# Kernel optimization log

Hardware: AMD Instinct MI355X
Metric: run time of the kernel (lower is better)

Reference implementation:

```python
import jax, jax.numpy as jnp
import numpy as np

N = 50000
E = 800000
IN_F = 128
OUT_F = 128


def setup_inputs() -> dict:
    key = jax.random.key(0)
    k1, k2, k3, k4, k5 = jax.random.split(key, 5)
    x = jax.random.normal(k1, (N, IN_F), dtype=jnp.float32)
    # sparse adjacency as COO edge list: row = dst (aggregating node), col = src
    edge_index = jax.random.randint(k2, (2, E), 0, N, dtype=jnp.int64)
    edge_weight = jax.random.uniform(k3, (E,), dtype=jnp.float32)
    # nn.Linear(in_features, out_features): W is [out, in], b is [out]
    W = jax.random.normal(k4, (OUT_F, IN_F), dtype=jnp.float32) * (1.0 / np.sqrt(IN_F))
    b = jax.random.normal(k5, (OUT_F,), dtype=jnp.float32) * 0.01
    return {"x": x, "edge_index": edge_index, "edge_weight": edge_weight, "W": W, "b": b}


def reference(x, edge_index, edge_weight, W, b):
    # hidden = self.linear(x)  -> [N, out]
    hidden = jnp.einsum("ni,oi->no", x, W) + b
    # out = adj @ hidden (SpMM): out[dst] += w_e * hidden[src]
    dst = edge_index[0]
    src = edge_index[1]
    msgs = edge_weight[:, None] * hidden[src]  # [E, out]
    out = jax.ops.segment_sum(msgs, dst, num_segments=x.shape[0])
    return out
```

## Files before the change

kernel.cpp:

```cpp
#include <hip/hip_runtime.h>
#include <hip/hip_bf16.h>

#define N_NODES 50000
#define N_EDGES 800000
#define FEAT    128
#define N_TILES (N_NODES / 16)
#define MAXD    32
#define OVF_CAP 16384
#define NODES_PER_GRP 6250
#define CHUNK   2048
#define NCHUNK  ((N_EDGES + CHUNK - 1) / CHUNK)

using short8  = __attribute__((ext_vector_type(8))) short;
using float4v = __attribute__((ext_vector_type(4))) float;


__device__ __forceinline__ unsigned short f2b(float f) {
    __hip_bfloat16 h = __float2bfloat16(f);
    return __builtin_bit_cast(unsigned short, h);
}

__global__ void k_init(const int* __restrict__ ei, int* __restrict__ flag,
                       int* __restrict__ fill) {
    int i = blockIdx.x * blockDim.x + threadIdx.x;
    if (i < N_NODES) fill[i] = 0;
    if (blockIdx.x == 0 && threadIdx.x < 64) {
        unsigned long long m = __ballot(ei[2 * threadIdx.x + 1] != 0);
        if (threadIdx.x == 0) { flag[0] = (m == 0ULL) ? 1 : 0; flag[1] = 0; }
    }
}

__global__ __launch_bounds__(256) void k_gemm(const float* __restrict__ x,
                                              const float* __restrict__ W,
                                              const float* __restrict__ bias,
                                              unsigned short* __restrict__ hidden) {
    __shared__ __align__(16) unsigned short Wlds[128 * 136];

    const int t = threadIdx.x;
    for (int j = 0; j < 16; ++j) {
        int idx4 = j * 256 + t;
        float4v wv = *(const float4v*)(W + (size_t)idx4 * 4);
        int r = (idx4 * 4) >> 7;
        int c = (idx4 * 4) & 127;
        unsigned short* p = &Wlds[r * 136 + c];
        p[0] = f2b(wv[0]); p[1] = f2b(wv[1]); p[2] = f2b(wv[2]); p[3] = f2b(wv[3]);
    }
    __syncthreads();

    const int wave = t >> 6;
    const int lane = t & 63;
    int tile = blockIdx.x * 4 + wave;
    if (tile >= N_TILES) tile = N_TILES - 1;
    const int rowBase = tile * 16;
    const int m    = lane & 15;
    const int quad = lane >> 4;

    float4v acc[8];
    for (int i = 0; i < 8; ++i) acc[i] = (float4v){0.f, 0.f, 0.f, 0.f};

    for (int kk = 0; kk < 4; ++kk) {
        const int k0 = kk * 32 + quad * 8;
        const float* ap = x + (size_t)(rowBase + m) * FEAT + k0;
        float4v a0 = *(const float4v*)(ap);
        float4v a1 = *(const float4v*)(ap + 4);
        short8 af;
        for (int j = 0; j < 4; ++j) { af[j] = (short)f2b(a0[j]); af[4 + j] = (short)f2b(a1[j]); }
        for (int nt = 0; nt < 8; ++nt) {
            short8 bf = *(const short8*)&Wlds[(nt * 16 + m) * 136 + k0];
            acc[nt] = __builtin_amdgcn_mfma_f32_16x16x32_bf16(af, bf, acc[nt], 0, 0, 0);
        }
    }

    const int r0 = rowBase + quad * 4;
    for (int nt = 0; nt < 8; ++nt) {
        const int col = nt * 16 + m;
        const float bc = bias[col];
        for (int r = 0; r < 4; ++r) {
            hidden[(size_t)(r0 + r) * FEAT + col] = f2b(acc[nt][r] + bc);
        }
    }
}

__global__ __launch_bounds__(256) void k_scatter(const int* __restrict__ ei,
                                                 const float* __restrict__ wt,
                                                 const int* __restrict__ flag,
                                                 int* __restrict__ fill,
                                                 unsigned int* __restrict__ slots,
                                                 int2* __restrict__ ovf) {
    const int grp = blockIdx.x & 7;
    const int lo  = grp * NODES_PER_GRP;
    const int hi  = lo + NODES_PER_GRP;
    const int sh  = flag[0];
    const int e0  = (blockIdx.x >> 3) * CHUNK + threadIdx.x;

    for (int i = 0; i < CHUNK / 256; ++i) {
        int e = e0 + i * 256;
        if (e >= N_EDGES) break;
        int dst = ei[(size_t)e << sh];
        if ((unsigned)dst >= N_NODES) dst = 0;
        if (dst < lo || dst >= hi) continue;
        int src = ei[(size_t)(N_EDGES + e) << sh];
        if ((unsigned)src >= N_NODES) src = 0;
        unsigned int rec = ((unsigned int)f2b(wt[e]) << 16) | (unsigned int)src;
        int pos = atomicAdd(&fill[dst], 1);
        if (pos < MAXD) {
            slots[(size_t)dst * MAXD + pos] = rec;
        } else {
            int op = atomicAdd((int*)&((int*)flag)[1], 1);
            if (op < OVF_CAP) { int2 r; r.x = dst; r.y = (int)rec; ovf[op] = r; }
        }
    }
}

__global__ __launch_bounds__(256) void k_agg(const int* __restrict__ fill,
                                             const unsigned int* __restrict__ slots,
                                             const unsigned int* __restrict__ hid,
                                             float* __restrict__ out) {
    const int wave = threadIdx.x >> 6;
    const int lane = threadIdx.x & 63;
    const int node = blockIdx.x * 4 + wave;
    if (node >= N_NODES) return;

    int deg = fill[node];
    if (deg > MAXD) deg = MAXD;
    const unsigned int* sl = slots + (size_t)node * MAXD;

    float a0 = 0.f, a1 = 0.f;

    int e = 0;
    for (; e + 4 <= deg; e += 4) {
        unsigned r0 = sl[e];
        unsigned r1 = sl[e + 1];
        unsigned r2 = sl[e + 2];
        unsigned r3 = sl[e + 3];
        unsigned h0 = hid[(size_t)(r0 & 0xffffu) * 64 + lane];
        unsigned h1 = hid[(size_t)(r1 & 0xffffu) * 64 + lane];
        unsigned h2 = hid[(size_t)(r2 & 0xffffu) * 64 + lane];
        unsigned h3 = hid[(size_t)(r3 & 0xffffu) * 64 + lane];
        float w0 = __uint_as_float(r0 & 0xffff0000u);
        float w1 = __uint_as_float(r1 & 0xffff0000u);
        float w2 = __uint_as_float(r2 & 0xffff0000u);
        float w3 = __uint_as_float(r3 & 0xffff0000u);
        a0 = fmaf(w0, __uint_as_float((h0 & 0xffffu) << 16), a0);
        a1 = fmaf(w0, __uint_as_float(h0 & 0xffff0000u), a1);
        a0 = fmaf(w1, __uint_as_float((h1 & 0xffffu) << 16), a0);
        a1 = fmaf(w1, __uint_as_float(h1 & 0xffff0000u), a1);
        a0 = fmaf(w2, __uint_as_float((h2 & 0xffffu) << 16), a0);
        a1 = fmaf(w2, __uint_as_float(h2 & 0xffff0000u), a1);
        a0 = fmaf(w3, __uint_as_float((h3 & 0xffffu) << 16), a0);
        a1 = fmaf(w3, __uint_as_float(h3 & 0xffff0000u), a1);
    }
    for (; e < deg; ++e) {
        unsigned r = sl[e];
        unsigned h = hid[(size_t)(r & 0xffffu) * 64 + lane];
        float w = __uint_as_float(r & 0xffff0000u);
        a0 = fmaf(w, __uint_as_float((h & 0xffffu) << 16), a0);
        a1 = fmaf(w, __uint_as_float(h & 0xffff0000u), a1);
    }

    *(float2*)(out + (size_t)node * FEAT + lane * 2) = make_float2(a0, a1);
}

__global__ __launch_bounds__(256) void k_ovf(const int* __restrict__ flag,
                                             const int2* __restrict__ ovf,
                                             const unsigned int* __restrict__ hid,
                                             float* __restrict__ out) {
    const int wave = threadIdx.x >> 6;
    const int lane = threadIdx.x & 63;
    int n = flag[1];
    if (n > OVF_CAP) n = OVF_CAP;
    for (int i = wave; i < n; i += 4) {
        int2 r = ovf[i];
        unsigned rec = (unsigned)r.y;
        float w = __uint_as_float(rec & 0xffff0000u);
        unsigned h = hid[(size_t)(rec & 0xffffu) * 64 + lane];
        float* o = out + (size_t)r.x * FEAT + lane * 2;
        atomicAdd(o,     w * __uint_as_float((h & 0xffffu) << 16));
        atomicAdd(o + 1, w * __uint_as_float(h & 0xffff0000u));
    }
}

extern "C" void kernel_launch(void* const* d_in, const int* in_sizes, int n_in,
                              void* d_out, int out_size, void* d_ws, size_t ws_size,
                              hipStream_t stream) {
    const float* x  = (const float*)d_in[0];
    const int*   ei = (const int*)d_in[1];
    const float* ew = (const float*)d_in[2];
    const float* W  = (const float*)d_in[3];
    const float* b  = (const float*)d_in[4];
    float* out = (float*)d_out;

    int*  flag = (int*)d_ws;
    int*  fill = flag + 16;
    int2* ovf  = (int2*)(fill + 50048);
    unsigned int* slots = (unsigned int*)(ovf + OVF_CAP);
    unsigned short* hidden = (unsigned short*)(slots + (size_t)N_NODES * MAXD);

    k_init   <<<(N_NODES + 255) / 256, 256, 0, stream>>>(ei, flag, fill);
    k_gemm   <<<(N_TILES + 3) / 4, 256, 0, stream>>>(x, W, b, hidden);
    k_scatter<<<NCHUNK * 8, 256, 0, stream>>>(ei, ew, flag, fill, slots, ovf);
    k_agg    <<<(N_NODES + 3) / 4, 256, 0, stream>>>(fill, slots, (const unsigned int*)hidden, out);
    k_ovf    <<<1, 256, 0, stream>>>(flag, ovf, (const unsigned int*)hidden, out);
}
```

Baseline: 176.4 us.

## Fuse GEMM with edge scatter, vectorize aggregation and fold overflow into it

Runs the bf16 MFMA linear layer and the CSR-slot scatter as disjoint block ranges of one kernel, so they run concurrently and a launch is saved. The scatter now batches its dst-index loads ahead of the atomic loop. The aggregation kernel splits each wave into four 16-lane groups that each handle one edge with 16-byte hidden-row loads, then reduces across groups with shuffles. Overflow edges are handled inside the aggregation by nodes whose degree exceeds the slot cap, which scans the whole overflow list and removes the separate atomic overflow kernel. This adds cost per high-degree node and reads slot records in 4-wide vectors beyond deg.

```diff
diff --git a/kernel.cpp b/kernel.cpp
--- a/kernel.cpp
+++ b/kernel.cpp
@@ -5,6 +5,7 @@
 #define N_EDGES 800000
 #define FEAT    128
 #define N_TILES (N_NODES / 16)
+#define GEMM_BLOCKS 784
 #define MAXD    32
 #define OVF_CAP 16384
 #define NODES_PER_GRP 6250
@@ -30,84 +31,93 @@
     }
 }
 
-__global__ __launch_bounds__(256) void k_gemm(const float* __restrict__ x,
-                                              const float* __restrict__ W,
-                                              const float* __restrict__ bias,
-                                              unsigned short* __restrict__ hidden) {
+__global__ __launch_bounds__(256) void k_fused(const float* __restrict__ x,
+                                               const float* __restrict__ W,
+                                               const float* __restrict__ bias,
+                                               unsigned short* __restrict__ hidden,
+                                               const int* __restrict__ ei,
+                                               const float* __restrict__ wt,
+                                               int* __restrict__ flag,
+                                               int* __restrict__ fill,
+                                               unsigned int* __restrict__ slots,
+                                               int2* __restrict__ ovf) {
     __shared__ __align__(16) unsigned short Wlds[128 * 136];
-
     const int t = threadIdx.x;
-    for (int j = 0; j < 16; ++j) {
-        int idx4 = j * 256 + t;
-        float4v wv = *(const float4v*)(W + (size_t)idx4 * 4);
-        int r = (idx4 * 4) >> 7;
-        int c = (idx4 * 4) & 127;
-        unsigned short* p = &Wlds[r * 136 + c];
-        p[0] = f2b(wv[0]); p[1] = f2b(wv[1]); p[2] = f2b(wv[2]); p[3] = f2b(wv[3]);
-    }
-    __syncthreads();
-
-    const int wave = t >> 6;
-    const int lane = t & 63;
-    int tile = blockIdx.x * 4 + wave;
-    if (tile >= N_TILES) tile = N_TILES - 1;
-    const int rowBase = tile * 16;
-    const int m    = lane & 15;
-    const int quad = lane >> 4;
-
-    float4v acc[8];
-    for (int i = 0; i < 8; ++i) acc[i] = (float4v){0.f, 0.f, 0.f, 0.f};
-
-    for (int kk = 0; kk < 4; ++kk) {
-        const int k0 = kk * 32 + quad * 8;
-        const float* ap = x + (size_t)(rowBase + m) * FEAT + k0;
-        float4v a0 = *(const float4v*)(ap);
-        float4v a1 = *(const float4v*)(ap + 4);
-        short8 af;
-        for (int j = 0; j < 4; ++j) { af[j] = (short)f2b(a0[j]); af[4 + j] = (short)f2b(a1[j]); }
+
+    if (blockIdx.x < GEMM_BLOCKS) {
+        for (int j = 0; j < 16; ++j) {
+            int idx4 = j * 256 + t;
+            float4v wv = *(const float4v*)(W + (size_t)idx4 * 4);
+            int r = (idx4 * 4) >> 7;
+            int c = (idx4 * 4) & 127;
+            unsigned short* p = &Wlds[r * 136 + c];
+            p[0] = f2b(wv[0]); p[1] = f2b(wv[1]); p[2] = f2b(wv[2]); p[3] = f2b(wv[3]);
+        }
+        __syncthreads();
+
+        const int wave = t >> 6;
+        const int lane = t & 63;
+        int tile = blockIdx.x * 4 + wave;
+        if (tile >= N_TILES) tile = N_TILES - 1;
+        const int rowBase = tile * 16;
+        const int m    = lane & 15;
+        const int quad = lane >> 4;
+
+        float4v acc[8];
+        for (int i = 0; i < 8; ++i) acc[i] = (float4v){0.f, 0.f, 0.f, 0.f};
+
+        for (int kk = 0; kk < 4; ++kk) {
+            const int k0 = kk * 32 + quad * 8;
+            const float* ap = x + (size_t)(rowBase + m) * FEAT + k0;
+            float4v a0 = *(const float4v*)(ap);
+            float4v a1 = *(const float4v*)(ap + 4);
+            short8 af;
+            for (int j = 0; j < 4; ++j) { af[j] = (short)f2b(a0[j]); af[4 + j] = (short)f2b(a1[j]); }
+            for (int nt = 0; nt < 8; ++nt) {
+                short8 bf = *(const short8*)&Wlds[(nt * 16 + m) * 136 + k0];
+                acc[nt] = __builtin_amdgcn_mfma_f32_16x16x32_bf16(af, bf, acc[nt], 0, 0, 0);
+            }
+        }
+
+        const int r0 = rowBase + quad * 4;
         for (int nt = 0; nt < 8; ++nt) {
-            short8 bf = *(const short8*)&Wlds[(nt * 16 + m) * 136 + k0];
-            acc[nt] = __builtin_amdgcn_mfma_f32_16x16x32_bf16(af, bf, acc[nt], 0, 0, 0);
-        }
-    }
-
-    const int r0 = rowBase + quad * 4;
-    for (int nt = 0; nt < 8; ++nt) {
-        const int col = nt * 16 + m;
-        const float bc = bias[col];
-        for (int r = 0; r < 4; ++r) {
-            hidden[(size_t)(r0 + r) * FEAT + col] = f2b(acc[nt][r] + bc);
-        }
-    }
-}
-
-__global__ __launch_bounds__(256) void k_scatter(const int* __restrict__ ei,
-                                                 const float* __restrict__ wt,
-                                                 const int* __restrict__ flag,
-                                                 int* __restrict__ fill,
-                                                 unsigned int* __restrict__ slots,
-                                                 int2* __restrict__ ovf) {
-    const int grp = blockIdx.x & 7;
-    const int lo  = grp * NODES_PER_GRP;
-    const int hi  = lo + NODES_PER_GRP;
-    const int sh  = flag[0];
-    const int e0  = (blockIdx.x >> 3) * CHUNK + threadIdx.x;
-
-    for (int i = 0; i < CHUNK / 256; ++i) {
-        int e = e0 + i * 256;
-        if (e >= N_EDGES) break;
-        int dst = ei[(size_t)e << sh];
-        if ((unsigned)dst >= N_NODES) dst = 0;
-        if (dst < lo || dst >= hi) continue;
-        int src = ei[(size_t)(N_EDGES + e) << sh];
-        if ((unsigned)src >= N_NODES) src = 0;
-        unsigned int rec = ((unsigned int)f2b(wt[e]) << 16) | (unsigned int)src;
-        int pos = atomicAdd(&fill[dst], 1);
-        if (pos < MAXD) {
-            slots[(size_t)dst * MAXD + pos] = rec;
-        } else {
-            int op = atomicAdd((int*)&((int*)flag)[1], 1);
-            if (op < OVF_CAP) { int2 r; r.x = dst; r.y = (int)rec; ovf[op] = r; }
+            const int col = nt * 16 + m;
+            const float bc = bias[col];
+            for (int r = 0; r < 4; ++r) {
+                hidden[(size_t)(r0 + r) * FEAT + col] = f2b(acc[nt][r] + bc);
+            }
+        }
+    } else {
+        const int bid = blockIdx.x - GEMM_BLOCKS;
+        const int grp = bid & 7;
+        const int lo  = grp * NODES_PER_GRP;
+        const int hi  = lo + NODES_PER_GRP;
+        const int sh  = flag[0];
+        const int e0  = (bid >> 3) * CHUNK + t;
+
+        int dsts[8];
+        #pragma unroll
+        for (int i = 0; i < 8; ++i) {
+            int e = e0 + i * 256;
+            dsts[i] = (e < N_EDGES) ? ei[(size_t)e << sh] : -1;
+        }
+        #pragma unroll
+        for (int i = 0; i < 8; ++i) {
+            int e = e0 + i * 256;
+            if (e >= N_EDGES) continue;
+            int dst = dsts[i];
+            if ((unsigned)dst >= N_NODES) dst = 0;
+            if (dst < lo || dst >= hi) continue;
+            int src = ei[(size_t)(N_EDGES + e) << sh];
+            if ((unsigned)src >= N_NODES) src = 0;
+            unsigned int rec = ((unsigned int)f2b(wt[e]) << 16) | (unsigned int)src;
+            int pos = atomicAdd(&fill[dst], 1);
+            if (pos < MAXD) {
+                slots[(size_t)dst * MAXD + pos] = rec;
+            } else {
+                int op = atomicAdd(&flag[1], 1);
+                if (op < OVF_CAP) { int2 r; r.x = dst; r.y = (int)rec; ovf[op] = r; }
+            }
         }
     }
 }
@@ -115,68 +125,73 @@
 __global__ __launch_bounds__(256) void k_agg(const int* __restrict__ fill,
                                              const unsigned int* __restrict__ slots,
                                              const unsigned int* __restrict__ hid,
+                                             const int* __restrict__ flag,
+                                             const int2* __restrict__ ovf,
                                              float* __restrict__ out) {
     const int wave = threadIdx.x >> 6;
     const int lane = threadIdx.x & 63;
     const int node = blockIdx.x * 4 + wave;
-    if (node >= N_NODES) return;
-
-    int deg = fill[node];
-    if (deg > MAXD) deg = MAXD;
+    const int grp  = lane >> 4;
+    const int sub  = lane & 15;
+
+    const int degf = fill[node];
+    const int deg  = (degf > MAXD) ? MAXD : degf;
     const unsigned int* sl = slots + (size_t)node * MAXD;
 
-    float a0 = 0.f, a1 = 0.f;
-
-    int e = 0;
-    for (; e + 4 <= deg; e += 4) {
-        unsigned r0 = sl[e];
-        unsigned r1 = sl[e + 1];
-        unsigned r2 = sl[e + 2];
-        unsigned r3 = sl[e + 3];
-        unsigned h0 = hid[(size_t)(r0 & 0xffffu) * 64 + lane];
-        unsigned h1 = hid[(size_t)(r1 & 0xffffu) * 64 + lane];
-        unsigned h2 = hid[(size_t)(r2 & 0xffffu) * 64 + lane];
-        unsigned h3 = hid[(size_t)(r3 & 0xffffu) * 64 + lane];
-        float w0 = __uint_as_float(r0 & 0xffff0000u);
-        float w1 = __uint_as_float(r1 & 0xffff0000u);
-        float w2 = __uint_as_float(r2 & 0xffff0000u);
-        float w3 = __uint_as_float(r3 & 0xffff0000u);
-        a0 = fmaf(w0, __uint_as_float((h0 & 0xffffu) << 16), a0);
-        a1 = fmaf(w0, __uint_as_float(h0 & 0xffff0000u), a1);
-        a0 = fmaf(w1, __uint_as_float((h1 & 0xffffu) << 16), a0);
-        a1 = fmaf(w1, __uint_as_float(h1 & 0xffff0000u), a1);
-        a0 = fmaf(w2, __uint_as_float((h2 & 0xffffu) << 16), a0);
-        a1 = fmaf(w2, __uint_as_float(h2 & 0xffff0000u), a1);
-        a0 = fmaf(w3, __uint_as_float((h3 & 0xffffu) << 16), a0);
-        a1 = fmaf(w3, __uint_as_float(h3 & 0xffff0000u), a1);
-    }
-    for (; e < deg; ++e) {
-        unsigned r = sl[e];
-        unsigned h = hid[(size_t)(r & 0xffffu) * 64 + lane];
-        float w = __uint_as_float(r & 0xffff0000u);
-        a0 = fmaf(w, __uint_as_float((h & 0xffffu) << 16), a0);
-        a1 = fmaf(w, __uint_as_float(h & 0xffff0000u), a1);
-    }
-
-    *(float2*)(out + (size_t)node * FEAT + lane * 2) = make_float2(a0, a1);
-}
-
-__global__ __launch_bounds__(256) void k_ovf(const int* __restrict__ flag,
-                                             const int2* __restrict__ ovf,
-                                             const unsigned int* __restrict__ hid,
-                                             float* __restrict__ out) {
-    const int wave = threadIdx.x >> 6;
-    const int lane = threadIdx.x & 63;
-    int n = flag[1];
-    if (n > OVF_CAP) n = OVF_CAP;
-    for (int i = wave; i < n; i += 4) {
-        int2 r = ovf[i];
-        unsigned rec = (unsigned)r.y;
-        float w = __uint_as_float(rec & 0xffff0000u);
-        unsigned h = hid[(size_t)(rec & 0xffffu) * 64 + lane];
-        float* o = out + (size_t)r.x * FEAT + lane * 2;
-        atomicAdd(o,     w * __uint_as_float((h & 0xffffu) << 16));
-        atomicAdd(o + 1, w * __uint_as_float(h & 0xffff0000u));
+    float acc[8];
+    #pragma unroll
+    for (int j = 0; j < 8; ++j) acc[j] = 0.f;
+
+    for (int e = 0; e < deg; e += 4) {
+        uint4 recs = *(const uint4*)(sl + e);
+        unsigned rec = (grp < 2) ? (grp == 0 ? recs.x : recs.y)
+                                 : (grp == 2 ? recs.z : recs.w);
+        const bool v = (e + grp) < deg;
+        const float w = v ? __uint_as_float(rec & 0xffff0000u) : 0.f;
+        const unsigned src = v ? (rec & 0xffffu) : 0u;
+        uint4 h = *((const uint4*)(hid + (size_t)src * 64) + sub);
+        acc[0] = fmaf(w, __uint_as_float((h.x & 0xffffu) << 16), acc[0]);
+        acc[1] = fmaf(w, __uint_as_float(h.x & 0xffff0000u),     acc[1]);
+        acc[2] = fmaf(w, __uint_as_float((h.y & 0xffffu) << 16), acc[2]);
+        acc[3] = fmaf(w, __uint_as_float(h.y & 0xffff0000u),     acc[3]);
+        acc[4] = fmaf(w, __uint_as_float((h.z & 0xffffu) << 16), acc[4]);
+        acc[5] = fmaf(w, __uint_as_float(h.z & 0xffff0000u),     acc[5]);
+        acc[6] = fmaf(w, __uint_as_float((h.w & 0xffffu) << 16), acc[6]);
+        acc[7] = fmaf(w, __uint_as_float(h.w & 0xffff0000u),     acc[7]);
+    }
+
+    if (degf > MAXD) {
+        int n = flag[1]; if (n > OVF_CAP) n = OVF_CAP;
+        for (int i = 0; i < n; ++i) {
+            int2 r = ovf[i];
+            if (r.x != node || (i & 3) != grp) continue;
+            unsigned rec = (unsigned)r.y;
+            float w = __uint_as_float(rec & 0xffff0000u);
+            unsigned src = rec & 0xffffu;
+            uint4 h = *((const uint4*)(hid + (size_t)src * 64) + sub);
+            acc[0] = fmaf(w, __uint_as_float((h.x & 0xffffu) << 16), acc[0]);
+            acc[1] = fmaf(w, __uint_as_float(h.x & 0xffff0000u),     acc[1]);
+            acc[2] = fmaf(w, __uint_as_float((h.y & 0xffffu) << 16), acc[2]);
+            acc[3] = fmaf(w, __uint_as_float(h.y & 0xffff0000u),     acc[3]);
+            acc[4] = fmaf(w, __uint_as_float((h.z & 0xffffu) << 16), acc[4]);
+            acc[5] = fmaf(w, __uint_as_float(h.z & 0xffff0000u),     acc[5]);
+            acc[6] = fmaf(w, __uint_as_float((h.w & 0xffffu) << 16), acc[6]);
+            acc[7] = fmaf(w, __uint_as_float(h.w & 0xffff0000u),     acc[7]);
+        }
+    }
+
+    #pragma unroll
+    for (int j = 0; j < 8; ++j) {
+        float a = acc[j];
+        a += __shfl_xor(a, 16, 64);
+        a += __shfl_xor(a, 32, 64);
+        acc[j] = a;
+    }
+
+    if (lane < 16) {
+        float* o = out + (size_t)node * FEAT + sub * 8;
+        *(float4*)(o)     = make_float4(acc[0], acc[1], acc[2], acc[3]);
+        *(float4*)(o + 4) = make_float4(acc[4], acc[5], acc[6], acc[7]);
     }
 }
 
@@ -196,9 +211,9 @@
     unsigned int* slots = (unsigned int*)(ovf + OVF_CAP);
     unsigned short* hidden = (unsigned short*)(slots + (size_t)N_NODES * MAXD);
 
-    k_init   <<<(N_NODES + 255) / 256, 256, 0, stream>>>(ei, flag, fill);
-    k_gemm   <<<(N_TILES + 3) / 4, 256, 0, stream>>>(x, W, b, hidden);
-    k_scatter<<<NCHUNK * 8, 256, 0, stream>>>(ei, ew, flag, fill, slots, ovf);
-    k_agg    <<<(N_NODES + 3) / 4, 256, 0, stream>>>(fill, slots, (const unsigned int*)hidden, out);
-    k_ovf    <<<1, 256, 0, stream>>>(flag, ovf, (const unsigned int*)hidden, out);
-}
+    k_init <<<(N_NODES + 255) / 256, 256, 0, stream>>>(ei, flag, fill);
+    k_fused<<<GEMM_BLOCKS + NCHUNK * 8, 256, 0, stream>>>(x, W, b, hidden, ei, ew,
+                                                          flag, fill, slots, ovf);
+    k_agg  <<<N_NODES / 4, 256, 0, stream>>>(fill, slots, (const unsigned int*)hidden,
+                                             flag, ovf, out);
+}
```

After: 173.3 us. Within noise of the previous version (-1.7%).
